# Optimization experiments

Hardware: AMD Instinct MI355X
Metric: run time of the kernel (lower is better)

The kernel has to match this reference:

```python
import jax, jax.numpy as jnp
import numpy as np

B, S, D, H = 4, 2048, 1024, 16
DK = D // H

def setup_inputs() -> dict:
    key = jax.random.key(0)
    ks = jax.random.split(key, 11)
    s = 1.0 / np.sqrt(D)
    return {
        "query": jax.random.normal(ks[0], (B, S, D), jnp.float32),
        "key_": jax.random.normal(ks[1], (B, S, D), jnp.float32),
        "value": jax.random.normal(ks[2], (B, S, D), jnp.float32),
        "Wq": jax.random.uniform(ks[3], (D, D), jnp.float32, -s, s),
        "bq": jax.random.uniform(ks[4], (D,), jnp.float32, -s, s),
        "Wk": jax.random.uniform(ks[5], (D, D), jnp.float32, -s, s),
        "bk": jax.random.uniform(ks[6], (D,), jnp.float32, -s, s),
        "Wv": jax.random.uniform(ks[7], (D, D), jnp.float32, -s, s),
        "bv": jax.random.uniform(ks[8], (D,), jnp.float32, -s, s),
        "Wo": jax.random.uniform(ks[9], (D, D), jnp.float32, -s, s),
        "bo": jax.random.uniform(ks[10], (D,), jnp.float32, -s, s),
    }

def _split_heads(x):
    # [B,S,D] -> [B,H,S,DK]
    b, s, _ = x.shape
    return x.reshape(b, s, H, DK).transpose(0, 2, 1, 3)

def reference(query, key_, value, Wq, bq, Wk, bk, Wv, bv, Wo, bo):
    Q = _split_heads(query @ Wq.T + bq)
    K = _split_heads(key_ @ Wk.T + bk)
    V = _split_heads(value @ Wv.T + bv)
    scores = jnp.einsum('bhqd,bhkd->bhqk', Q, K) / np.sqrt(DK).astype(np.float32)
    attn = jax.nn.softmax(scores, axis=-1)
    ctx = jnp.einsum('bhqk,bhkd->bhqd', attn, V)  # [B,H,S,DK]
    ctx = ctx.transpose(0, 2, 1, 3).reshape(query.shape[0], -1, D)
    return ctx @ Wo.T + bo
```

## Files before the change

### kernel.cpp

```cpp
#include <hip/hip_runtime.h>
#include <hip/hip_bf16.h>
#include <math.h>


#define B_SZ   4
#define S_LEN  2048
#define D_DIM  1024
#define NH     16
#define DKD    64
#define M_TOT  (B_SZ * S_LEN)

typedef __bf16 bf16_t;
typedef bf16_t bf16x8 __attribute__((ext_vector_type(8)));
typedef bf16_t bf16x4 __attribute__((ext_vector_type(4)));
typedef float  f32x4  __attribute__((ext_vector_type(4)));

typedef __attribute__((address_space(1))) void gvoid;
typedef __attribute__((address_space(3))) void lvoid;

extern "C" __device__ float __ocml_native_exp2_f32(float);

__global__ __launch_bounds__(256)
void cvt3_kernel(const float* __restrict__ s0, const float* __restrict__ s1,
                 const float* __restrict__ s2, bf16_t* __restrict__ d0,
                 bf16_t* __restrict__ d1, bf16_t* __restrict__ d2, int n4)
{
    const float* src = (blockIdx.z == 0) ? s0 : (blockIdx.z == 1) ? s1 : s2;
    bf16_t*      dst = (blockIdx.z == 0) ? d0 : (blockIdx.z == 1) ? d1 : d2;
    const int i = blockIdx.x * blockDim.x + threadIdx.x;
    if (i < n4) {
        f32x4 v = *(const f32x4*)(src + (size_t)i * 4);
        bf16x4 o;
        #pragma unroll
        for (int j = 0; j < 4; ++j) o[j] = (bf16_t)v[j];
        *(bf16x4*)(dst + (size_t)i * 4) = o;
    }
}

__global__ __launch_bounds__(256)
void cvt_kernel(const float* __restrict__ src, bf16_t* __restrict__ dst, int n4)
{
    const int i = blockIdx.x * blockDim.x + threadIdx.x;
    if (i < n4) {
        f32x4 v = *(const f32x4*)(src + (size_t)i * 4);
        bf16x4 o;
        #pragma unroll
        for (int j = 0; j < 4; ++j) o[j] = (bf16_t)v[j];
        *(bf16x4*)(dst + (size_t)i * 4) = o;
    }
}

__global__ __launch_bounds__(256, 3)
void qkv_gemm(const float* __restrict__ Aq, const float* __restrict__ Ak,
              const float* __restrict__ Av,
              const bf16_t* __restrict__ Wqb, const bf16_t* __restrict__ Wkb,
              const bf16_t* __restrict__ Wvb,
              const float* __restrict__ bq, const float* __restrict__ bk,
              const float* __restrict__ bv,
              bf16_t* __restrict__ Qw, bf16_t* __restrict__ Kw,
              bf16_t* __restrict__ Vt, float qscale)
{
    constexpr int K = 1024, N = 1024;
    constexpr int BM = 128, BK = 64;
    constexpr int NT = K / BK;

    __shared__ __align__(16) bf16_t lA[2][BM * 32];
    __shared__ __align__(16) bf16_t lB[2][2][128 * 32];

    const int z = blockIdx.z;
    const float* A  = (z == 0) ? Aq : (z == 1) ? Ak : Av;
    const bf16_t* W = (z == 0) ? Wqb : (z == 1) ? Wkb : Wvb;
    const float* bias = (z == 0) ? bq : (z == 1) ? bk : bv;
    const float scale = (z == 0) ? qscale : 1.0f;

    const int tid  = threadIdx.x;
    const int wave = tid >> 6;
    const int lane = tid & 63;

    const int row0 = blockIdx.x * BM;
    const int col0 = blockIdx.y * 128;

    const int wr = (wave >> 1) * 64;
    const int wc = (wave & 1) * 64;

    f32x4 acc[4][4] = {};

    const int frow = lane & 15;
    const int kq   = (lane >> 4) * 8;

    const int arow = tid >> 3;
    const int ak8  = (tid & 7) * 8;
    const int asub = (tid >> 2) & 1;
    const int akk  = (tid & 3) * 8;

    auto stageB = [&](int k0s, int bufi) {
        #pragma unroll
        for (int s = 0; s < 2; ++s)
            #pragma unroll
            for (int c2 = 0; c2 < 2; ++c2) {
                const int chunk = c2 * 4 + wave;
                const int e     = chunk * 512 + lane * 8;
                const int rr    = e >> 5;
                const int kk    = e & 31;
                __builtin_amdgcn_global_load_lds(
                    (gvoid*)(W + (size_t)(col0 + rr) * K + k0s + 32 * s + kk),
                    (lvoid*)(&lB[bufi][s][chunk * 512]), 16, 0, 0);
            }
    };

    stageB(0, 0);

    f32x4 pa[4][2];
    #pragma unroll
    for (int p = 0; p < 4; ++p) {
        const float* g = A + (size_t)(row0 + p * 32 + arow) * K + ak8;
        pa[p][0] = *(const f32x4*)g;
        pa[p][1] = *(const f32x4*)(g + 4);
    }

    for (int t = 0; t < NT; ++t) {
        const int k0  = t * BK;
        const int buf = t & 1;

        if (t + 1 < NT) stageB(k0 + BK, buf ^ 1);

        #pragma unroll
        for (int p = 0; p < 4; ++p) {
            bf16x8 a8;
            #pragma unroll
            for (int j = 0; j < 4; ++j) {
                a8[j]     = (bf16_t)pa[p][0][j];
                a8[4 + j] = (bf16_t)pa[p][1][j];
            }
            *(bf16x8*)(&lA[asub][(p * 32 + arow) * 32 + akk]) = a8;
        }

        if (t + 1 < NT)
            asm volatile("s_waitcnt vmcnt(4) lgkmcnt(0)" ::: "memory");
        else
            asm volatile("s_waitcnt vmcnt(0) lgkmcnt(0)" ::: "memory");
        __builtin_amdgcn_s_barrier();

        if (t + 1 < NT) {
            #pragma unroll
            for (int p = 0; p < 4; ++p) {
                const float* g = A + (size_t)(row0 + p * 32 + arow) * K + (k0 + BK) + ak8;
                pa[p][0] = *(const f32x4*)g;
                pa[p][1] = *(const f32x4*)(g + 4);
            }
        }

        #pragma unroll
        for (int s = 0; s < 2; ++s) {
            bf16x8 af[4], bfr[4];
            #pragma unroll
            for (int i = 0; i < 4; ++i) {
                af[i]  = *(const bf16x8*)(&lA[s][(wr + i * 16 + frow) * 32 + kq]);
                bfr[i] = *(const bf16x8*)(&lB[buf][s][(wc + i * 16 + frow) * 32 + kq]);
            }
            #pragma unroll
            for (int i = 0; i < 4; ++i)
                #pragma unroll
                for (int j = 0; j < 4; ++j)
                    acc[i][j] = __builtin_amdgcn_mfma_f32_16x16x32_bf16(af[i], bfr[j], acc[i][j], 0, 0, 0);
        }

        asm volatile("" ::: "memory");
        __builtin_amdgcn_s_barrier();
    }

    const int rb   = (lane >> 4) * 4;
    const int ccol = lane & 15;
    #pragma unroll
    for (int j = 0; j < 4; ++j) {
        const int n = col0 + wc + j * 16 + ccol;
        const float bvv = bias[n];
        #pragma unroll
        for (int i = 0; i < 4; ++i) {
            const int m = row0 + wr + i * 16 + rb;
            if (z == 2) {
                bf16x4 o4;
                #pragma unroll
                for (int r = 0; r < 4; ++r) o4[r] = (bf16_t)(acc[i][j][r] + bvv);
                *(bf16x4*)(Vt + (size_t)n * M_TOT + m) = o4;
            } else {
                bf16_t* Cp = (z == 0) ? Qw : Kw;
                #pragma unroll
                for (int r = 0; r < 4; ++r)
                    Cp[(size_t)(m + r) * N + n] = (bf16_t)((acc[i][j][r] + bvv) * scale);
            }
        }
    }
}

__global__ __launch_bounds__(256, 2)
void gemm_out(const bf16_t* __restrict__ A, const bf16_t* __restrict__ Bt,
              const float* __restrict__ bias, float* __restrict__ C)
{
    constexpr int K = 1024, N = 1024;
    constexpr int BM = 128, BK = 64;
    constexpr int NT = K / BK;

    __shared__ __align__(16) bf16_t lA[2][2][BM * 32];
    __shared__ __align__(16) bf16_t lB[2][2][128 * 32];

    const int tid  = threadIdx.x;
    const int wave = tid >> 6;
    const int lane = tid & 63;

    const int row0 = blockIdx.x * BM;
    const int col0 = blockIdx.y * 128;

    const int wr = (wave >> 1) * 64;
    const int wc = (wave & 1) * 64;

    f32x4 acc[4][4] = {};

    const int frow = lane & 15;
    const int kq   = (lane >> 4) * 8;

    auto stage = [&](int k0s, int bufi) {
        #pragma unroll
        for (int s = 0; s < 2; ++s)
            #pragma unroll
            for (int c2 = 0; c2 < 2; ++c2) {
                const int chunk = c2 * 4 + wave;
                const int e     = chunk * 512 + lane * 8;
                const int r     = e >> 5;
                const int kk    = e & 31;
                __builtin_amdgcn_global_load_lds(
                    (gvoid*)(A + (size_t)(row0 + r) * K + k0s + 32 * s + kk),
                    (lvoid*)(&lA[bufi][s][chunk * 512]), 16, 0, 0);
                __builtin_amdgcn_global_load_lds(
                    (gvoid*)(Bt + (size_t)(col0 + r) * K + k0s + 32 * s + kk),
                    (lvoid*)(&lB[bufi][s][chunk * 512]), 16, 0, 0);
            }
    };

    stage(0, 0);

    for (int t = 0; t < NT; ++t) {
        const int buf = t & 1;

        if (t + 1 < NT) {
            stage((t + 1) * BK, buf ^ 1);
            asm volatile("s_waitcnt vmcnt(8)" ::: "memory");
        } else {
            asm volatile("s_waitcnt vmcnt(0)" ::: "memory");
        }
        __builtin_amdgcn_s_barrier();

        #pragma unroll
        for (int s = 0; s < 2; ++s) {
            bf16x8 af[4], bfr[4];
            #pragma unroll
            for (int i = 0; i < 4; ++i) {
                af[i]  = *(const bf16x8*)(&lA[buf][s][(wr + i * 16 + frow) * 32 + kq]);
                bfr[i] = *(const bf16x8*)(&lB[buf][s][(wc + i * 16 + frow) * 32 + kq]);
            }
            #pragma unroll
            for (int i = 0; i < 4; ++i)
                #pragma unroll
                for (int j = 0; j < 4; ++j)
                    acc[i][j] = __builtin_amdgcn_mfma_f32_16x16x32_bf16(af[i], bfr[j], acc[i][j], 0, 0, 0);
        }

        asm volatile("" ::: "memory");
        __builtin_amdgcn_s_barrier();
    }

    const int rb   = (lane >> 4) * 4;
    const int ccol = lane & 15;
    #pragma unroll
    for (int j = 0; j < 4; ++j) {
        const int n = col0 + wc + j * 16 + ccol;
        const float bvv = bias[n];
        #pragma unroll
        for (int i = 0; i < 4; ++i) {
            const int m = row0 + wr + i * 16 + rb;
            #pragma unroll
            for (int r = 0; r < 4; ++r)
                C[(size_t)(m + r) * N + n] = acc[i][j][r] + bvv;
        }
    }
}

__global__ __launch_bounds__(256, 2)
void attn_mfma(const bf16_t* __restrict__ Qg, const bf16_t* __restrict__ Kg,
               const bf16_t* __restrict__ Vt, bf16_t* __restrict__ ctx)
{
    constexpr int PSTR = 72;
    __shared__ __align__(16) bf16_t lK[64 * PSTR];
    __shared__ __align__(16) bf16_t lV[64 * PSTR];
    __shared__ __align__(16) bf16_t lP[4][64 * PSTR];

    const int tid  = threadIdx.x;
    const int wave = tid >> 6;
    const int lane = tid & 63;
    const int qd   = lane >> 4;
    const int c    = lane & 15;

    const int g    = blockIdx.x;
    const int bh   = ((g >> 6) << 3) | (g & 7);
    const int qblk = (g >> 3) & 7;
    const int b    = bh >> 4;
    const int h    = bh & 15;

    const int q0 = qblk * 256 + wave * 64;

    const bf16_t* Qb = Qg + ((size_t)(b * S_LEN + q0)) * D_DIM + h * DKD;
    const bf16_t* Kb = Kg + ((size_t)(b * S_LEN)) * D_DIM + h * DKD;
    const bf16_t* Vb = Vt + ((size_t)(h * DKD)) * M_TOT + b * S_LEN;

    bf16_t* Pw = &lP[wave][0];

    bf16x8 qf[4][2];
    #pragma unroll
    for (int qt = 0; qt < 4; ++qt)
        #pragma unroll
        for (int ks = 0; ks < 2; ++ks)
            qf[qt][ks] = *(const bf16x8*)(Qb + (size_t)(qt * 16 + c) * D_DIM + ks * 32 + qd * 8);

    bf16x8 ones;
    #pragma unroll
    for (int i = 0; i < 8; ++i) ones[i] = (bf16_t)1.0f;

    f32x4 oacc[4][4] = {};
    f32x4 lacc[4]    = {};

    const int srow = tid >> 3;
    const int sc8  = (tid & 7) * 8;

    bf16x8 kv[2], vv[2];
    #pragma unroll
    for (int cc = 0; cc < 2; ++cc) {
        const int row = cc * 32 + srow;
        kv[cc] = *(const bf16x8*)(Kb + (size_t)row * D_DIM + sc8);
        vv[cc] = *(const bf16x8*)(Vb + (size_t)row * M_TOT + sc8);
    }

    for (int kt = 0; kt < S_LEN; kt += 64) {
        __syncthreads();
        #pragma unroll
        for (int cc = 0; cc < 2; ++cc) {
            const int row = cc * 32 + srow;
            *(bf16x8*)(lK + row * PSTR + sc8) = kv[cc];
            *(bf16x8*)(lV + row * PSTR + sc8) = vv[cc];
        }
        __syncthreads();

        if (kt + 64 < S_LEN) {
            #pragma unroll
            for (int cc = 0; cc < 2; ++cc) {
                const int row = cc * 32 + srow;
                kv[cc] = *(const bf16x8*)(Kb + (size_t)(kt + 64 + row) * D_DIM + sc8);
                vv[cc] = *(const bf16x8*)(Vb + (size_t)row * M_TOT + kt + 64 + sc8);
            }
        }

        bf16x8 kf[4][2];
        #pragma unroll
        for (int i = 0; i < 4; ++i)
            #pragma unroll
            for (int ks = 0; ks < 2; ++ks)
                kf[i][ks] = *(const bf16x8*)(lK + (i * 16 + c) * PSTR + ks * 32 + qd * 8);

        #pragma unroll
        for (int qh = 0; qh < 2; ++qh) {
            f32x4 st[4][2] = {};
            __builtin_amdgcn_s_setprio(1);
            #pragma unroll
            for (int ks = 0; ks < 2; ++ks)
                #pragma unroll
                for (int i = 0; i < 4; ++i)
                    #pragma unroll
                    for (int qt = 0; qt < 2; ++qt)
                        st[i][qt] = __builtin_amdgcn_mfma_f32_16x16x32_bf16(
                            kf[i][ks], qf[qh * 2 + qt][ks], st[i][qt], 0, 0, 0);
            __builtin_amdgcn_s_setprio(0);

            #pragma unroll
            for (int i = 0; i < 4; ++i)
                #pragma unroll
                for (int qt = 0; qt < 2; ++qt) {
                    bf16x4 pw;
                    #pragma unroll
                    for (int r = 0; r < 4; ++r)
                        pw[r] = (bf16_t)__ocml_native_exp2_f32(st[i][qt][r]);
                    *(bf16x4*)(Pw + ((qh * 2 + qt) * 16 + c) * PSTR + i * 16 + qd * 4) = pw;
                }
        }

        bf16x8 vf[4][2];
        #pragma unroll
        for (int fm = 0; fm < 4; ++fm)
            #pragma unroll
            for (int ks = 0; ks < 2; ++ks)
                vf[fm][ks] = *(const bf16x8*)(lV + (fm * 16 + c) * PSTR + ks * 32 + qd * 8);

        __builtin_amdgcn_s_setprio(1);
        #pragma unroll
        for (int qn = 0; qn < 4; ++qn)
            #pragma unroll
            for (int ks = 0; ks < 2; ++ks) {
                bf16x8 pf = *(const bf16x8*)(Pw + (qn * 16 + c) * PSTR + ks * 32 + qd * 8);
                lacc[qn] = __builtin_amdgcn_mfma_f32_16x16x32_bf16(ones, pf, lacc[qn], 0, 0, 0);
                #pragma unroll
                for (int fm = 0; fm < 4; ++fm)
                    oacc[fm][qn] = __builtin_amdgcn_mfma_f32_16x16x32_bf16(vf[fm][ks], pf, oacc[fm][qn], 0, 0, 0);
            }
        __builtin_amdgcn_s_setprio(0);
    }

    #pragma unroll
    for (int qn = 0; qn < 4; ++qn) {
        const float linv = 1.0f / lacc[qn][0];
        bf16_t* op = ctx + ((size_t)(b * S_LEN + q0 + qn * 16 + c)) * D_DIM + h * DKD + qd * 4;
        #pragma unroll
        for (int fm = 0; fm < 4; ++fm) {
            bf16x4 o4;
            #pragma unroll
            for (int r = 0; r < 4; ++r) o4[r] = (bf16_t)(oacc[fm][qn][r] * linv);
            *(bf16x4*)(op + fm * 16) = o4;
        }
    }
}

extern "C" void kernel_launch(void* const* d_in, const int* in_sizes, int n_in,
                              void* d_out, int out_size, void* d_ws, size_t ws_size,
                              hipStream_t stream)
{
    const float* query = (const float*)d_in[0];
    const float* key_  = (const float*)d_in[1];
    const float* value = (const float*)d_in[2];
    const float* Wq    = (const float*)d_in[3];
    const float* bq    = (const float*)d_in[4];
    const float* Wk    = (const float*)d_in[5];
    const float* bk    = (const float*)d_in[6];
    const float* Wv    = (const float*)d_in[7];
    const float* bv    = (const float*)d_in[8];
    const float* Wo    = (const float*)d_in[9];
    const float* bo    = (const float*)d_in[10];
    float* out = (float*)d_out;

    const size_t mat  = (size_t)M_TOT * D_DIM;
    const size_t wmat = (size_t)D_DIM * D_DIM;

    bf16_t* t0 = (bf16_t*)d_ws;
    bf16_t* w0 = t0 + mat;
    bf16_t* Qw = w0 + wmat;
    bf16_t* Kw = Qw + mat;
    bf16_t* Vt = Kw + mat;
    bf16_t* w1 = t0;
    bf16_t* w2 = t0 + wmat;

    const int gcvt_w = (int)(wmat / 4 / 256);
    const float qscale = 0.18033688011112042f;

    cvt3_kernel<<<dim3(gcvt_w, 1, 3), 256, 0, stream>>>(Wq, Wk, Wv, w0, w1, w2,
                                                        (int)(wmat / 4));

    qkv_gemm<<<dim3(M_TOT / 128, D_DIM / 128, 3), 256, 0, stream>>>(
        query, key_, value, w0, w1, w2, bq, bk, bv, Qw, Kw, Vt, qscale);

    cvt_kernel<<<gcvt_w, 256, 0, stream>>>(Wo, w0, (int)(wmat / 4));

    attn_mfma<<<dim3(B_SZ * NH * (S_LEN / 256)), 256, 0, stream>>>(Qw, Kw, Vt, t0);

    gemm_out<<<dim3(M_TOT / 128, D_DIM / 128), 256, 0, stream>>>(t0, w0, bo, out);
}
```

Baseline: 330.9 us.

## Restructure output GEMM into 256x256 tiles with 8 waves and phased prefetch

The output projection GEMM moves from 128x128 tiles with 4 waves to 256x256 tiles with 8 waves. LDS uses an XOR-swizzled 64-wide K layout to avoid bank conflicts. Next-tile loads are split into four phases interleaved with MFMA sub-blocks, with s_setprio around the math. The aim is more operand reuse per loaded byte and better overlap of loads with compute. The cost is more accumulator registers and only 128 blocks, which may underfill the GPU.

```diff
diff --git a/kernel.cpp b/kernel.cpp
--- a/kernel.cpp
+++ b/kernel.cpp
@@ -193,96 +193,145 @@
     }
 }
 
-__global__ __launch_bounds__(256, 2)
+__global__ __launch_bounds__(512, 2)
 void gemm_out(const bf16_t* __restrict__ A, const bf16_t* __restrict__ Bt,
               const float* __restrict__ bias, float* __restrict__ C)
 {
     constexpr int K = 1024, N = 1024;
-    constexpr int BM = 128, BK = 64;
+    constexpr int BM = 256, BK = 64;
     constexpr int NT = K / BK;
 
-    __shared__ __align__(16) bf16_t lA[2][2][BM * 32];
-    __shared__ __align__(16) bf16_t lB[2][2][128 * 32];
+    __shared__ __align__(16) bf16_t lA[2][BM * BK];
+    __shared__ __align__(16) bf16_t lB[2][BM * BK];
 
     const int tid  = threadIdx.x;
     const int wave = tid >> 6;
     const int lane = tid & 63;
 
     const int row0 = blockIdx.x * BM;
-    const int col0 = blockIdx.y * 128;
-
-    const int wr = (wave >> 1) * 64;
-    const int wc = (wave & 1) * 64;
-
-    f32x4 acc[4][4] = {};
+    const int col0 = blockIdx.y * BM;
+
+    const int wr = (wave >> 2) * 128;
+    const int wc = (wave & 3) * 64;
+
+    f32x4 acc[8][4] = {};
 
     const int frow = lane & 15;
-    const int kq   = (lane >> 4) * 8;
-
-    auto stage = [&](int k0s, int bufi) {
-        #pragma unroll
-        for (int s = 0; s < 2; ++s)
-            #pragma unroll
-            for (int c2 = 0; c2 < 2; ++c2) {
-                const int chunk = c2 * 4 + wave;
-                const int e     = chunk * 512 + lane * 8;
-                const int r     = e >> 5;
-                const int kk    = e & 31;
-                __builtin_amdgcn_global_load_lds(
-                    (gvoid*)(A + (size_t)(row0 + r) * K + k0s + 32 * s + kk),
-                    (lvoid*)(&lA[bufi][s][chunk * 512]), 16, 0, 0);
-                __builtin_amdgcn_global_load_lds(
-                    (gvoid*)(Bt + (size_t)(col0 + r) * K + k0s + 32 * s + kk),
-                    (lvoid*)(&lB[bufi][s][chunk * 512]), 16, 0, 0);
-            }
+    const int qd   = lane >> 4;
+    const int fr7  = frow & 7;
+
+    auto stage_half = [&](int k0s, int bufi, int h) {
+        const bf16_t* G = (h < 2) ? A : Bt;
+        bf16_t* L = (h < 2) ? &lA[bufi][0] : &lB[bufi][0];
+        const int base0 = (h < 2) ? row0 : col0;
+        const int rbase = (h & 1) * 128;
+        const int gs    = ((lane & 7) ^ ((lane >> 3) & 7)) * 8;
+        #pragma unroll
+        for (int l = 0; l < 2; ++l) {
+            const int rchunk = rbase + l * 64 + wave * 8;
+            const int rloc   = rchunk + (lane >> 3);
+            __builtin_amdgcn_global_load_lds(
+                (gvoid*)(G + (size_t)(base0 + rloc) * K + k0s + gs),
+                (lvoid*)(L + (size_t)rchunk * 64), 16, 0, 0);
+        }
     };
 
-    stage(0, 0);
-
-    for (int t = 0; t < NT; ++t) {
-        const int buf = t & 1;
-
-        if (t + 1 < NT) {
-            stage((t + 1) * BK, buf ^ 1);
-            asm volatile("s_waitcnt vmcnt(8)" ::: "memory");
-        } else {
-            asm volatile("s_waitcnt vmcnt(0)" ::: "memory");
-        }
+#define GOUT_PHASE(PH, MH, NH, VCSTR)                                          \
+    do {                                                                       \
+        stage_half(k1, bufn, PH);                                              \
+        asm volatile("s_waitcnt vmcnt(" VCSTR ")" ::: "memory");               \
+        __builtin_amdgcn_s_barrier();                                          \
+        bf16x8 af[4][2], bfr[2][2];                                            \
+        _Pragma("unroll")                                                      \
+        for (int ks = 0; ks < 2; ++ks) {                                       \
+            const int kg = ((ks * 4 + qd) ^ fr7) * 8;                          \
+            _Pragma("unroll")                                                  \
+            for (int mf = 0; mf < 4; ++mf)                                     \
+                af[mf][ks] = *(const bf16x8*)(&lA[buf][(size_t)(wr + ((MH)*4 + mf) * 16 + frow) * 64 + kg]); \
+            _Pragma("unroll")                                                  \
+            for (int nf = 0; nf < 2; ++nf)                                     \
+                bfr[nf][ks] = *(const bf16x8*)(&lB[buf][(size_t)(wc + ((NH)*2 + nf) * 16 + frow) * 64 + kg]); \
+        }                                                                      \
+        __builtin_amdgcn_s_setprio(1);                                         \
+        _Pragma("unroll")                                                      \
+        for (int ks = 0; ks < 2; ++ks)                                         \
+            _Pragma("unroll")                                                  \
+            for (int mf = 0; mf < 4; ++mf)                                     \
+                _Pragma("unroll")                                              \
+                for (int nf = 0; nf < 2; ++nf)                                 \
+                    acc[(MH)*4 + mf][(NH)*2 + nf] =                            \
+                        __builtin_amdgcn_mfma_f32_16x16x32_bf16(               \
+                            af[mf][ks], bfr[nf][ks],                           \
+                            acc[(MH)*4 + mf][(NH)*2 + nf], 0, 0, 0);           \
+        __builtin_amdgcn_s_setprio(0);                                         \
+    } while (0)
+
+#define GOUT_EPI(MH, NH)                                                       \
+    do {                                                                       \
+        bf16x8 af[4][2], bfr[2][2];                                            \
+        _Pragma("unroll")                                                      \
+        for (int ks = 0; ks < 2; ++ks) {                                       \
+            const int kg = ((ks * 4 + qd) ^ fr7) * 8;                          \
+            _Pragma("unroll")                                                  \
+            for (int mf = 0; mf < 4; ++mf)                                     \
+                af[mf][ks] = *(const bf16x8*)(&lA[buf][(size_t)(wr + ((MH)*4 + mf) * 16 + frow) * 64 + kg]); \
+            _Pragma("unroll")                                                  \
+            for (int nf = 0; nf < 2; ++nf)                                     \
+                bfr[nf][ks] = *(const bf16x8*)(&lB[buf][(size_t)(wc + ((NH)*2 + nf) * 16 + frow) * 64 + kg]); \
+        }                                                                      \
+        _Pragma("unroll")                                                      \
+        for (int ks = 0; ks < 2; ++ks)                                         \
+            _Pragma("unroll")                                                  \
+            for (int mf = 0; mf < 4; ++mf)                                     \
+                _Pragma("unroll")                                              \
+                for (int nf = 0; nf < 2; ++nf)                                 \
+                    acc[(MH)*4 + mf][(NH)*2 + nf] =                            \
+                        __builtin_amdgcn_mfma_f32_16x16x32_bf16(               \
+                            af[mf][ks], bfr[nf][ks],                           \
+                            acc[(MH)*4 + mf][(NH)*2 + nf], 0, 0, 0);           \
+    } while (0)
+
+    #pragma unroll
+    for (int h = 0; h < 4; ++h) stage_half(0, 0, h);
+
+    #pragma unroll 1
+    for (int t = 0; t < NT - 1; ++t) {
+        const int buf  = t & 1;
+        const int bufn = buf ^ 1;
+        const int k1   = (t + 1) * BK;
+        GOUT_PHASE(0, 0, 0, "2");
+        GOUT_PHASE(1, 0, 1, "4");
+        GOUT_PHASE(2, 1, 0, "6");
+        GOUT_PHASE(3, 1, 1, "8");
         __builtin_amdgcn_s_barrier();
-
-        #pragma unroll
-        for (int s = 0; s < 2; ++s) {
-            bf16x8 af[4], bfr[4];
-            #pragma unroll
-            for (int i = 0; i < 4; ++i) {
-                af[i]  = *(const bf16x8*)(&lA[buf][s][(wr + i * 16 + frow) * 32 + kq]);
-                bfr[i] = *(const bf16x8*)(&lB[buf][s][(wc + i * 16 + frow) * 32 + kq]);
-            }
-            #pragma unroll
-            for (int i = 0; i < 4; ++i)
-                #pragma unroll
-                for (int j = 0; j < 4; ++j)
-                    acc[i][j] = __builtin_amdgcn_mfma_f32_16x16x32_bf16(af[i], bfr[j], acc[i][j], 0, 0, 0);
-        }
-
-        asm volatile("" ::: "memory");
+    }
+
+    {
+        const int buf = (NT - 1) & 1;
+        asm volatile("s_waitcnt vmcnt(0)" ::: "memory");
         __builtin_amdgcn_s_barrier();
+        GOUT_EPI(0, 0);
+        GOUT_EPI(0, 1);
+        GOUT_EPI(1, 0);
+        GOUT_EPI(1, 1);
     }
 
     const int rb   = (lane >> 4) * 4;
     const int ccol = lane & 15;
     #pragma unroll
-    for (int j = 0; j < 4; ++j) {
-        const int n = col0 + wc + j * 16 + ccol;
+    for (int nf = 0; nf < 4; ++nf) {
+        const int n = col0 + wc + nf * 16 + ccol;
         const float bvv = bias[n];
         #pragma unroll
-        for (int i = 0; i < 4; ++i) {
-            const int m = row0 + wr + i * 16 + rb;
+        for (int mf = 0; mf < 8; ++mf) {
+            const int m = row0 + wr + mf * 16 + rb;
             #pragma unroll
             for (int r = 0; r < 4; ++r)
-                C[(size_t)(m + r) * N + n] = acc[i][j][r] + bvv;
-        }
-    }
+                C[(size_t)(m + r) * N + n] = acc[mf][nf][r] + bvv;
+        }
+    }
+#undef GOUT_PHASE
+#undef GOUT_EPI
 }
 
 __global__ __launch_bounds__(256, 2)
@@ -467,5 +516,5 @@
 
     attn_mfma<<<dim3(B_SZ * NH * (S_LEN / 256)), 256, 0, stream>>>(Qw, Kw, Vt, t0);
 
-    gemm_out<<<dim3(M_TOT / 128, D_DIM / 128), 256, 0, stream>>>(t0, w0, bo, out);
+    gemm_out<<<dim3(M_TOT / 256, D_DIM / 256), 512, 0, stream>>>(t0, w0, bo, out);
 }
```

Result: slower. 344.3 us (+4.0%).
